# Optimization experiments

Measured on AMD Instinct MI355X. Metric: run time of the kernel, lower is better.

Reference implementation:

```python
import jax, jax.numpy as jnp
import numpy as np

L = 8  # kernel_size
OUT_CHA = 256


def _pm_full(r, L, trm):
    # Faithful numpy port of PM_Full_creation (row order matters for PCM matching)
    tnpm = [np.arange(L)[:, None]]
    npm_r = tnpm[0]
    for _ in range(r - 1):
        nc = npm_r.shape[1]
        blocks = []
        for j in range(1, L - nc + 1):
            np_r = (npm_r[:, nc - 1] + j)[:, None]
            keep = np.where(np_r[:, 0] < L)[0]
            blocks.append(np.concatenate([npm_r[keep], np_r[keep]], axis=1))
        npm_r = np.vstack(blocks)
        tnpm.append(npm_r)
    return np.vstack([np.repeat(tnpm[len(t) - 1], np.asarray(t), axis=1) for t in trm])


def _pcm0(pm2, pm3):
    # PCM_creation(...)[0]: col 0 of PM3, plus row index in PM2 matching cols 1:
    pos = np.array([np.where((pm2 == row).all(axis=1))[0][0] for row in pm3[:, 1:]])
    return np.stack([pm3[:, 0], pos], axis=1)


def _indices():
    pm2 = _pm_full(2, L, [[2], [1, 1]])
    pm3 = _pm_full(3, L, [[3], [1, 2], [2, 1], [1, 1, 1]])
    return pm2.astype(np.int32), _pcm0(pm2, pm3).astype(np.int32)


def setup_inputs() -> dict:
    key = jax.random.key(0)
    k1, k2, k3 = jax.random.split(key, 3)
    B, C, H, W = 4, 256, 56, 56
    pm2, pcm = _indices()
    h_ks = L + pm2.shape[0] + pcm.shape[0]          # 8 + 36 + 120 = 164
    in_exp = (C // L) * h_ks                        # 32 * 164 = 5248
    inp = jax.random.normal(k1, (B, C, H, W), dtype=jnp.float32)
    weight = jax.random.normal(k2, (OUT_CHA, in_exp), dtype=jnp.float32) * 0.02
    bias = jax.random.normal(k3, (OUT_CHA,), dtype=jnp.float32) * 0.01
    return {"input": inp, "weight": weight, "bias": bias,
            "pm2": jnp.asarray(pm2), "pcm": jnp.asarray(pcm)}


def reference(input, weight, bias, pm2, pcm):
    B, C, H, W = input.shape
    x = input.reshape(B, C // L, L, H, W)                     # (B, C/L, L, H, W)
    x2 = x[:, :, pm2[:, 0]] * x[:, :, pm2[:, 1]]              # second-order terms
    x3 = x[:, :, pcm[:, 0]] * x2[:, :, pcm[:, 1]]             # third-order terms
    xc = jnp.concatenate([x, x2, x3], axis=2)                 # (B, C/L, H_ks, H, W)
    xc = xc.reshape(B, -1, H, W)                              # (B, in_exp, H, W)
    out = jnp.einsum('bchw,oc->bohw', xc, weight)             # 1x1 conv, groups=1
    return out + bias[None, :, None, None]
```

## Files before the change

kernel.cpp:

```cpp
#include <hip/hip_runtime.h>
#include <stdint.h>


typedef short bf16x8 __attribute__((ext_vector_type(8)));
typedef float f32x4  __attribute__((ext_vector_type(4)));

__device__ __forceinline__ unsigned f2bf(float f) {
  unsigned u = __float_as_uint(f);
  return ((u + 0x7FFFu + ((u >> 16) & 1u)) >> 16) & 0xFFFFu;
}
__device__ __forceinline__ unsigned pk2(float lo, float hi) {
  return f2bf(lo) | (f2bf(hi) << 16);
}

#define ROW_S 200

constexpr int PI(int b, int c) { return 8 * b - b * (b - 1) / 2 + (c - b); }

struct CTab {
  unsigned char pa[36], pb[36];
  unsigned char ta[120], tb[120], tc3[120];
};
constexpr CTab gen_ctab() {
  CTab t{};
  int n = 0;
  for (int a = 0; a < 8; ++a)
    for (int b = a; b < 8; ++b) { t.pa[n] = (unsigned char)a; t.pb[n] = (unsigned char)b; ++n; }
  int m = 0;
  for (int a = 0; a < 8; ++a)
    for (int b = a; b < 8; ++b)
      for (int c = b; c < 8; ++c) {
        t.ta[m] = (unsigned char)a; t.tb[m] = (unsigned char)b; t.tc3[m] = (unsigned char)c; ++m;
      }
  return t;
}
constexpr CTab CT = gen_ctab();
__device__ const CTab dCT = CT;

template <int K>
__device__ __forceinline__ float featc(const float* __restrict__ x,
                                       const float* __restrict__ pr) {
  if constexpr (K < 8) {
    return x[K];
  } else if constexpr (K < 44) {
    return pr[K - 8];
  } else if constexpr (K < 164) {
    constexpr int r = K - 44;
    constexpr int a = CT.ta[r], b = CT.tb[r], c = CT.tc3[r];
    return x[a] * pr[PI(b, c)];
  } else {
    return 0.0f;
  }
}

template <int CH>
__device__ __forceinline__ void emit_chunk(const float* __restrict__ x,
                                           const float* __restrict__ pr,
                                           short* __restrict__ arow) {
  unsigned u0 = pk2(featc<CH * 8 + 0>(x, pr), featc<CH * 8 + 1>(x, pr));
  unsigned u1 = pk2(featc<CH * 8 + 2>(x, pr), featc<CH * 8 + 3>(x, pr));
  unsigned u2 = pk2(featc<CH * 8 + 4>(x, pr), featc<CH * 8 + 5>(x, pr));
  unsigned u3 = pk2(featc<CH * 8 + 6>(x, pr), featc<CH * 8 + 7>(x, pr));
  uint4 v; v.x = u0; v.y = u1; v.z = u2; v.w = u3;
  *reinterpret_cast<uint4*>(arow + (CH << 3)) = v;
}

__device__ __forceinline__ void stage_q0(const float* x, const float* pr, short* arow) {
  emit_chunk<0>(x, pr, arow);  emit_chunk<1>(x, pr, arow);  emit_chunk<2>(x, pr, arow);
  emit_chunk<3>(x, pr, arow);  emit_chunk<4>(x, pr, arow);  emit_chunk<5>(x, pr, arow);
}
__device__ __forceinline__ void stage_q1(const float* x, const float* pr, short* arow) {
  emit_chunk<6>(x, pr, arow);  emit_chunk<7>(x, pr, arow);  emit_chunk<8>(x, pr, arow);
  emit_chunk<9>(x, pr, arow);  emit_chunk<10>(x, pr, arow);
}
__device__ __forceinline__ void stage_q2(const float* x, const float* pr, short* arow) {
  emit_chunk<11>(x, pr, arow); emit_chunk<12>(x, pr, arow); emit_chunk<13>(x, pr, arow);
  emit_chunk<14>(x, pr, arow); emit_chunk<15>(x, pr, arow);
}
__device__ __forceinline__ void stage_q3(const float* x, const float* pr, short* arow) {
  emit_chunk<16>(x, pr, arow); emit_chunk<17>(x, pr, arow); emit_chunk<18>(x, pr, arow);
  emit_chunk<19>(x, pr, arow); emit_chunk<20>(x, pr, arow);
}

__device__ __forceinline__ void stage_dispatch(int part, const float* x,
                                               short* arow) {
  float pr[36];
#pragma unroll
  for (int a = 0; a < 8; ++a)
#pragma unroll
    for (int b = a; b < 8; ++b) pr[PI(a, b)] = x[a] * x[b];
  if      (part == 0) stage_q0(x, pr, arow);
  else if (part == 1) stage_q1(x, pr, arow);
  else if (part == 2) stage_q2(x, pr, arow);
  else                stage_q3(x, pr, arow);
}

__global__ void build_kmap(const int* __restrict__ pm2, const int* __restrict__ pcm,
                           int* __restrict__ kmapG) {
  __shared__ unsigned short rsig[164];
  const int tid = threadIdx.x;

  if (tid < 164) {
    unsigned s;
    if (tid < 8) {
      s = 1u << (2 * tid);
    } else if (tid < 44) {
      int q = tid - 8;
      s = (1u << (2 * pm2[2 * q])) + (1u << (2 * pm2[2 * q + 1]));
    } else {
      int r = tid - 44;
      int c0 = pcm[2 * r], pos = pcm[2 * r + 1];
      s = (1u << (2 * c0)) + (1u << (2 * pm2[2 * pos])) + (1u << (2 * pm2[2 * pos + 1]));
    }
    rsig[tid] = (unsigned short)s;
  }
  __syncthreads();

  if (tid < 192) {
    int kk = -1;
    if (tid < 164) {
      unsigned cs;
      if (tid < 8) {
        cs = 1u << (2 * tid);
      } else if (tid < 44) {
        int q = tid - 8;
        cs = (1u << (2 * dCT.pa[q])) + (1u << (2 * dCT.pb[q]));
      } else {
        int r = tid - 44;
        cs = (1u << (2 * dCT.ta[r])) + (1u << (2 * dCT.tb[r])) + (1u << (2 * dCT.tc3[r]));
      }
      for (int t = 0; t < 164; ++t)
        if (rsig[t] == (unsigned short)cs) { kk = t; break; }
    }
    kmapG[tid] = kk;
  }
}

__global__ void prep_w(const float* __restrict__ w, const int* __restrict__ kmapG,
                       short* __restrict__ wout) {
  __shared__ short kmap[192];
  const int tid = threadIdx.x;
  if (tid < 192) kmap[tid] = (short)kmapG[tid];
  __syncthreads();

  int e = blockIdx.x * 256 + tid;
  int j  = e & 7;
  int n  = (e >> 3) & 255;
  int t2 = e >> 11;
  int q  = t2 & 3;
  int sg = t2 >> 2;
  int g  = sg / 6;
  int s  = sg - g * 6;
  int kc = s * 32 + q * 8 + j;
  int kk = kmap[kc];
  float val = (kk >= 0) ? w[n * 5248 + g * 164 + kk] : 0.0f;
  wout[e] = (short)f2bf(val);
}

__global__ __launch_bounds__(256, 3) void poly_gemm(
    const float* __restrict__ in, const short* __restrict__ wbf,
    const float* __restrict__ bias, float* __restrict__ out) {
  __shared__ __align__(16) short ldsA[2][64 * ROW_S];

  const int tid  = threadIdx.x;
  const int m0   = blockIdx.x * 64;
  const int n0   = blockIdx.y * 128;
  const int lane = tid & 63;
  const int wave = tid >> 6;
  const int quad = lane >> 4;
  const int l16  = lane & 15;

  {
    uint4 z; z.x = 0u; z.y = 0u; z.z = 0u; z.w = 0u;
    for (int i = tid; i < 2 * 64 * 4; i += 256) {
      int b   = i >> 8;
      int rem = i & 255;
      int row = rem >> 2;
      int q4  = rem & 3;
      *reinterpret_cast<uint4*>(&ldsA[b][row * ROW_S + 168 + q4 * 8]) = z;
    }
  }

  f32x4 acc[4][2];
#pragma unroll
  for (int mf = 0; mf < 4; mf++)
#pragma unroll
    for (int nf = 0; nf < 2; nf++) acc[mf][nf] = (f32x4){0.f, 0.f, 0.f, 0.f};

  const unsigned bb = (unsigned)m0 / 3136u;
  const unsigned pp = (unsigned)m0 - bb * 3136u;
  const float* xbase = in + (size_t)bb * 802816u + pp + lane;

  float xr[8];
#pragma unroll
  for (int c = 0; c < 8; ++c) xr[c] = xbase[(size_t)c * 3136u];
  stage_dispatch(wave, xr, &ldsA[0][lane * ROW_S]);
#pragma unroll
  for (int c = 0; c < 8; ++c) xr[c] = xbase[(size_t)(8 + c) * 3136u];
  __syncthreads();

  int cur = 0;
  for (int g = 0; g < 32; ++g) {
    bf16x8 ball[6][2];
#pragma unroll
    for (int ks = 0; ks < 6; ++ks) {
      const int sg = g * 6 + ks;
#pragma unroll
      for (int nf = 0; nf < 2; ++nf) {
        int n = n0 + wave * 32 + nf * 16 + l16;
        ball[ks][nf] = *(const bf16x8*)(wbf + (((size_t)(sg * 4 + quad) * 256 + n) << 3));
      }
    }
    float xn[8];
    if (g + 2 < 32) {
      const float* xp = xbase + (size_t)((g + 2) * 8) * 3136u;
#pragma unroll
      for (int c = 0; c < 8; ++c) xn[c] = xp[(size_t)c * 3136u];
    }

    if (g + 1 < 32)
      stage_dispatch(wave, xr, &ldsA[cur ^ 1][lane * ROW_S]);

    const short* abuf = ldsA[cur];
#pragma unroll
    for (int ks = 0; ks < 6; ++ks) {
      bf16x8 af[4];
#pragma unroll
      for (int mf = 0; mf < 4; ++mf)
        af[mf] = *(const bf16x8*)(abuf + (mf * 16 + l16) * ROW_S + ks * 32 + quad * 8);
#pragma unroll
      for (int mf = 0; mf < 4; ++mf)
#pragma unroll
        for (int nf = 0; nf < 2; ++nf)
          acc[mf][nf] = __builtin_amdgcn_mfma_f32_16x16x32_bf16(af[mf], ball[ks][nf], acc[mf][nf], 0, 0, 0);
    }

    if (g + 2 < 32) {
#pragma unroll
      for (int c = 0; c < 8; ++c) xr[c] = xn[c];
    }
    cur ^= 1;
    __syncthreads();
  }

#pragma unroll
  for (int nf = 0; nf < 2; nf++) {
    const int col = n0 + wave * 32 + nf * 16 + l16;
    const float bv = bias[col];
#pragma unroll
    for (int mf = 0; mf < 4; mf++) {
#pragma unroll
      for (int r = 0; r < 4; r++) {
        unsigned p2 = pp + (unsigned)(mf * 16 + quad * 4 + r);
        out[(size_t)bb * 802816u + (size_t)col * 3136u + p2] = acc[mf][nf][r] + bv;
      }
    }
  }
}

extern "C" void kernel_launch(void* const* d_in, const int* in_sizes, int n_in,
                              void* d_out, int out_size, void* d_ws, size_t ws_size,
                              hipStream_t stream) {
  (void)in_sizes; (void)n_in; (void)out_size; (void)ws_size;
  const float* inp  = (const float*)d_in[0];
  const float* w    = (const float*)d_in[1];
  const float* bias = (const float*)d_in[2];
  const int*   pm2  = (const int*)d_in[3];
  const int*   pcm  = (const int*)d_in[4];
  int*   kmapG = (int*)d_ws;
  short* wbf   = (short*)((char*)d_ws + 1024);

  build_kmap<<<1, 256, 0, stream>>>(pm2, pcm, kmapG);
  prep_w<<<6144, 256, 0, stream>>>(w, kmapG, wbf);
  poly_gemm<<<dim3(196, 2), 256, 0, stream>>>(inp, wbf, bias, (float*)d_out);
}
```

Measured before the change: 149.9 us.

## Split GEMM K-dimension across two grid slices and vectorize weight prep

```diff
diff --git a/kernel.cpp b/kernel.cpp
--- a/kernel.cpp
+++ b/kernel.cpp
@@ -136,39 +136,47 @@
   }
 }
 
-__global__ void prep_w(const float* __restrict__ w, const int* __restrict__ kmapG,
-                       short* __restrict__ wout) {
-  __shared__ short kmap[192];
-  const int tid = threadIdx.x;
-  if (tid < 192) kmap[tid] = (short)kmapG[tid];
-  __syncthreads();
-
-  int e = blockIdx.x * 256 + tid;
-  int j  = e & 7;
-  int n  = (e >> 3) & 255;
-  int t2 = e >> 11;
+__global__ __launch_bounds__(256) void prep_w(const float* __restrict__ w,
+                                              const int* __restrict__ kmapG,
+                                              short* __restrict__ wout) {
+  int t  = blockIdx.x * 256 + threadIdx.x;
+  int n  = t & 255;
+  int t2 = t >> 8;
   int q  = t2 & 3;
   int sg = t2 >> 2;
   int g  = sg / 6;
   int s  = sg - g * 6;
-  int kc = s * 32 + q * 8 + j;
-  int kk = kmap[kc];
-  float val = (kk >= 0) ? w[n * 5248 + g * 164 + kk] : 0.0f;
-  wout[e] = (short)f2bf(val);
+  const float* wrow = w + (size_t)n * 5248u + g * 164;
+  unsigned v[8];
+#pragma unroll
+  for (int j = 0; j < 8; ++j) {
+    int kk = kmapG[s * 32 + q * 8 + j];
+    v[j] = (kk >= 0) ? f2bf(wrow[kk]) : 0u;
+  }
+  uint4 o;
+  o.x = v[0] | (v[1] << 16);
+  o.y = v[2] | (v[3] << 16);
+  o.z = v[4] | (v[5] << 16);
+  o.w = v[6] | (v[7] << 16);
+  *reinterpret_cast<uint4*>(wout + ((size_t)t << 3)) = o;
 }
 
 __global__ __launch_bounds__(256, 3) void poly_gemm(
     const float* __restrict__ in, const short* __restrict__ wbf,
-    const float* __restrict__ bias, float* __restrict__ out) {
+    const float* __restrict__ bias, float* __restrict__ out,
+    float* __restrict__ part, int kcount) {
   __shared__ __align__(16) short ldsA[2][64 * ROW_S];
 
-  const int tid  = threadIdx.x;
-  const int m0   = blockIdx.x * 64;
-  const int n0   = blockIdx.y * 128;
-  const int lane = tid & 63;
-  const int wave = tid >> 6;
-  const int quad = lane >> 4;
-  const int l16  = lane & 15;
+  const int tid   = threadIdx.x;
+  const int m0    = blockIdx.x * 64;
+  const int n0    = blockIdx.y * 128;
+  const int khalf = blockIdx.z;
+  const int kbase = khalf * kcount;
+  const int lane  = tid & 63;
+  const int wave  = tid >> 6;
+  const int quad  = lane >> 4;
+  const int l16   = lane & 15;
+  float* dst = khalf ? part : out;
 
   {
     uint4 z; z.x = 0u; z.y = 0u; z.z = 0u; z.w = 0u;
@@ -189,7 +197,8 @@
 
   const unsigned bb = (unsigned)m0 / 3136u;
   const unsigned pp = (unsigned)m0 - bb * 3136u;
-  const float* xbase = in + (size_t)bb * 802816u + pp + lane;
+  const float* xbase = in + (size_t)bb * 802816u + pp + lane
+                          + (size_t)(kbase * 8) * 3136u;
 
   float xr[8];
 #pragma unroll
@@ -200,7 +209,8 @@
   __syncthreads();
 
   int cur = 0;
-  for (int g = 0; g < 32; ++g) {
+  for (int gi = 0; gi < kcount; ++gi) {
+    const int g = kbase + gi;
     bf16x8 ball[6][2];
 #pragma unroll
     for (int ks = 0; ks < 6; ++ks) {
@@ -212,13 +222,13 @@
       }
     }
     float xn[8];
-    if (g + 2 < 32) {
-      const float* xp = xbase + (size_t)((g + 2) * 8) * 3136u;
+    if (gi + 2 < kcount) {
+      const float* xp = xbase + (size_t)((gi + 2) * 8) * 3136u;
 #pragma unroll
       for (int c = 0; c < 8; ++c) xn[c] = xp[(size_t)c * 3136u];
     }
 
-    if (g + 1 < 32)
+    if (gi + 1 < kcount)
       stage_dispatch(wave, xr, &ldsA[cur ^ 1][lane * ROW_S]);
 
     const short* abuf = ldsA[cur];
@@ -235,7 +245,7 @@
           acc[mf][nf] = __builtin_amdgcn_mfma_f32_16x16x32_bf16(af[mf], ball[ks][nf], acc[mf][nf], 0, 0, 0);
     }
 
-    if (g + 2 < 32) {
+    if (gi + 2 < kcount) {
 #pragma unroll
       for (int c = 0; c < 8; ++c) xr[c] = xn[c];
     }
@@ -246,22 +256,31 @@
 #pragma unroll
   for (int nf = 0; nf < 2; nf++) {
     const int col = n0 + wave * 32 + nf * 16 + l16;
-    const float bv = bias[col];
+    const float bv = (khalf == 0) ? bias[col] : 0.0f;
 #pragma unroll
     for (int mf = 0; mf < 4; mf++) {
 #pragma unroll
       for (int r = 0; r < 4; r++) {
         unsigned p2 = pp + (unsigned)(mf * 16 + quad * 4 + r);
-        out[(size_t)bb * 802816u + (size_t)col * 3136u + p2] = acc[mf][nf][r] + bv;
+        dst[(size_t)bb * 802816u + (size_t)col * 3136u + p2] = acc[mf][nf][r] + bv;
       }
     }
   }
+}
+
+__global__ __launch_bounds__(256) void reduce_add(float4* __restrict__ out,
+                                                  const float4* __restrict__ part) {
+  int i = blockIdx.x * 256 + threadIdx.x;
+  float4 a = out[i];
+  float4 b = part[i];
+  a.x += b.x; a.y += b.y; a.z += b.z; a.w += b.w;
+  out[i] = a;
 }
 
 extern "C" void kernel_launch(void* const* d_in, const int* in_sizes, int n_in,
                               void* d_out, int out_size, void* d_ws, size_t ws_size,
                               hipStream_t stream) {
-  (void)in_sizes; (void)n_in; (void)out_size; (void)ws_size;
+  (void)in_sizes; (void)n_in; (void)out_size;
   const float* inp  = (const float*)d_in[0];
   const float* w    = (const float*)d_in[1];
   const float* bias = (const float*)d_in[2];
@@ -269,8 +288,15 @@
   const int*   pcm  = (const int*)d_in[4];
   int*   kmapG = (int*)d_ws;
   short* wbf   = (short*)((char*)d_ws + 1024);
+  float* part  = (float*)((char*)d_ws + 1024 + 3145728);
+
+  const size_t need = 1024u + 3145728u + 12845056u;
+  const int nz = (ws_size >= need) ? 2 : 1;
+  const int kcount = 32 / nz;
 
   build_kmap<<<1, 256, 0, stream>>>(pm2, pcm, kmapG);
-  prep_w<<<6144, 256, 0, stream>>>(w, kmapG, wbf);
-  poly_gemm<<<dim3(196, 2), 256, 0, stream>>>(inp, wbf, bias, (float*)d_out);
-}
+  prep_w<<<768, 256, 0, stream>>>(w, kmapG, wbf);
+  poly_gemm<<<dim3(196, 2, nz), 256, 0, stream>>>(inp, wbf, bias, (float*)d_out, part, kcount);
+  if (nz == 2)
+    reduce_add<<<3136, 256, 0, stream>>>((float4*)d_out, (const float4*)part);
+}
```

Result: slower. 163.7 us (+9.2%).
